# Optimization experiments

Hardware: AMD Instinct MI355X
Metric: run time of the kernel (lower is better)

The kernel has to match this reference:

```python
import jax, jax.numpy as jnp
import numpy as np
from jax import lax

INPUT_SIZE = 512
STRIDES = (8, 16, 32)
NUM_CLASSES = 2
KA = 3  # anchors per scale
EPS = 1e-8
ANCHORS = np.array([[[10, 13], [16, 30], [33, 23]],
                    [[30, 61], [62, 45], [59, 119]],
                    [[116, 90], [156, 198], [373, 326]]], dtype=np.float32)

def _grid(stride):
    f = INPUT_SIZE // stride
    gy, gx = np.meshgrid(np.arange(f), np.arange(f), indexing='ij')
    return jnp.asarray(np.stack([gx, gy], -1).reshape(-1, 2).astype(np.float32))  # [HW,2] (x,y)

GRIDS = [_grid(s) for s in STRIDES]


def conv_ltc(x, conv_w, bn_gamma, bn_beta, cm, vleak, tau_m, e_revin):
    """Discrete LTC recurrence over time (tau_input=True, usetaum=True, stream_opt=True).
    x: [B,T,C,H,W] -> [B,T,Cout,H,W]"""
    B, T, C, H, W = x.shape
    Cout = conv_w.shape[0]

    def step(v_pre, xt):
        z = lax.conv_general_dilated(xt, conv_w, (1, 1), ((1, 1), (1, 1)),
                                     dimension_numbers=('NCHW', 'OIHW', 'NCHW'))
        wih = z * bn_gamma + bn_beta  # BatchNorm in eval form (per-channel affine)
        num = tau_m * v_pre / (vleak + cm * jax.nn.sigmoid(wih)) + wih * e_revin
        v = jax.nn.sigmoid(num / (1.0 + EPS))
        return v, v

    v0 = jnp.zeros((B, Cout, H, W), x.dtype)
    _, ys = lax.scan(step, v0, jnp.moveaxis(x, 1, 0))  # [T,B,Cout,H,W]
    return jnp.moveaxis(ys, 0, 1)


def head(y, w, b):
    # 1x1 conv detection head
    return jnp.einsum('bchw,oc->bohw', y, w) + b[None, :, None, None]


def decode_scale(pred, i):
    """pred: [B, KA*(1+C+4), h, w] -> obj [B,hw*KA,1], cls [B,hw*KA,C], box [B,hw*KA,4]."""
    B, _, h, w = pred.shape
    s = STRIDES[i]
    p = jnp.transpose(pred, (0, 2, 3, 1))  # [B,h,w,21]
    obj = p[..., :KA].reshape(B, -1, 1)
    cls = p[..., KA:KA * (1 + NUM_CLASSES)].reshape(B, -1, NUM_CLASSES)
    reg = p[..., KA * (1 + NUM_CLASSES):].reshape(B, h * w, KA, 4)
    anchors = jnp.asarray(ANCHORS[i])  # [KA,2]
    xy = (jax.nn.sigmoid(reg[..., :2]) + GRIDS[i][None, :, None, :]) * s
    wh = jnp.exp(reg[..., 2:]) * anchors[None, None, :, :]
    xywh = jnp.concatenate([xy, wh], -1).reshape(B, -1, 4)
    box = jnp.concatenate([xywh[..., :2] - xywh[..., 2:] * 0.5,
                           xywh[..., :2] + xywh[..., 2:] * 0.5], -1) / INPUT_SIZE
    return obj, cls, box


def setup_inputs() -> dict:
    key = jax.random.key(0)
    ks = jax.random.split(key, 12)
    B = 8
    x = jax.random.uniform(ks[0], (B, 5, 5, 512, 512), jnp.float32)
    y1 = jax.random.normal(ks[1], (B, 768, 16, 16), jnp.float32)
    y2 = jax.random.normal(ks[2], (B, 384, 32, 32), jnp.float32)
    y3 = jax.random.normal(ks[3], (B, 192, 64, 64), jnp.float32)
    conv_w = jax.random.normal(ks[4], (5, 5, 3, 3), jnp.float32) * 0.15  # xavier-ish
    bn_gamma = jnp.ones((5, 1, 1), jnp.float32)
    bn_beta = jnp.zeros((5, 1, 1), jnp.float32)
    cm = 1.0 + 0.1 * jax.random.normal(ks[5], (5, 1, 1), jnp.float32)
    vleak = 1.0 + 0.1 * jax.random.normal(ks[6], (5, 1, 1), jnp.float32)
    tau_m = 0.8 - 0.3 * jax.random.uniform(ks[7], (5, 1, 1), jnp.float32)
    e_revin = 1.0 + 0.1 * jax.random.normal(ks[8], (5, 1, 1), jnp.float32)
    OC = KA * (1 + NUM_CLASSES + 4)  # 21
    w1 = jax.random.normal(ks[9], (OC, 768), jnp.float32) * 0.02
    w2 = jax.random.normal(ks[10], (OC, 384), jnp.float32) * 0.02
    w3 = jax.random.normal(ks[11], (OC, 192), jnp.float32) * 0.02
    b1 = jnp.zeros((OC,), jnp.float32)
    b2 = jnp.zeros((OC,), jnp.float32)
    b3 = jnp.zeros((OC,), jnp.float32)
    return dict(x=x, y1=y1, y2=y2, y3=y3, conv_w=conv_w, bn_gamma=bn_gamma,
                bn_beta=bn_beta, cm=cm, vleak=vleak, tau_m=tau_m, e_revin=e_revin,
                w1=w1, b1=b1, w2=w2, b2=b2, w3=w3, b3=b3)


def reference(x, y1, y2, y3, conv_w, bn_gamma, bn_beta, cm, vleak, tau_m, e_revin,
              w1, b1, w2, b2, w3, b3):
    enc = conv_ltc(x, conv_w, bn_gamma, bn_beta, cm, vleak, tau_m, e_revin)
    # preds ordered [pred_s (y3, stride 8), pred_m (y2, 16), pred_l (y1, 32)]
    preds = [head(y3, w3, b3), head(y2, w2, b2), head(y1, w1, b1)]
    objs, clss, boxes = [], [], []
    for i, p in enumerate(preds):
        o, c, bx = decode_scale(p, i)
        objs.append(o); clss.append(c); boxes.append(bx)
    det = jnp.concatenate([jnp.concatenate(objs, 1),
                           jnp.concatenate(clss, 1),
                           jnp.concatenate(boxes, 1)], -1)  # [B, 16128, 7]
    return enc, det
```

## Files before the change

kernel.cpp:

```cpp
#include <hip/hip_runtime.h>
#include <math.h>

#define HH 512
#define WW 512
#define HWp (HH * WW)
#define TT 5
#define CC 5

#define CTW 64
#define CTH 16
#define NROW (CTH + 2)
#define GCOL 18
#define LCP (GCOL * 4)
#define LDSF (CC * NROW * LCP)
#define NG (CC * NROW * GCOL)
#define NBUF 3
#define SPARE_BYTES (NBUF * LDSF * 4)

#define NHEADB 672
#define NCONVB 2048

#define XS_FLOATS (NBUF * LDSF + 256)

typedef float v2f __attribute__((ext_vector_type(2)));

typedef __attribute__((address_space(3))) char       lds_char_t;
typedef __attribute__((address_space(1)))  const char glb_char_t;

__device__ __forceinline__ float fast_sigmoid(float x) {
    return __builtin_amdgcn_rcpf(1.0f + __expf(-x));
}

extern "C" __global__ __launch_bounds__(512, 4)
void spikefpn_fused(const float* __restrict__ x, const float* __restrict__ cw,
                    const float* __restrict__ gamma, const float* __restrict__ beta,
                    const float* __restrict__ cm, const float* __restrict__ vleak,
                    const float* __restrict__ tau, const float* __restrict__ erev,
                    const float* __restrict__ y3, const float* __restrict__ w3, const float* __restrict__ b3,
                    const float* __restrict__ y2, const float* __restrict__ w2, const float* __restrict__ b2,
                    const float* __restrict__ y1, const float* __restrict__ w1, const float* __restrict__ b1,
                    float* __restrict__ out, float* __restrict__ det)
{
    __shared__ float xs[XS_FLOATS];

    const int bid = blockIdx.x;
    const int tid = threadIdx.x;

    if (bid < NHEADB) {
        float* smem = xs;
        const float *y, *w, *bias;
        int Cin, f, lgf, lgchunks, row_off;
        float s;
        float aw0, aw1, aw2, ah0, ah1, ah2;
        int sb;

        if (bid < 512) {
            sb = bid;       y = y3; w = w3; bias = b3; Cin = 192; f = 64; lgf = 6; lgchunks = 6; s = 8.0f;  row_off = 0;
            aw0 = 10.f;  ah0 = 13.f;  aw1 = 16.f;  ah1 = 30.f;  aw2 = 33.f;  ah2 = 23.f;
        } else if (bid < 640) {
            sb = bid - 512; y = y2; w = w2; bias = b2; Cin = 384; f = 32; lgf = 5; lgchunks = 4; s = 16.0f; row_off = 12288;
            aw0 = 30.f;  ah0 = 61.f;  aw1 = 62.f;  ah1 = 45.f;  aw2 = 59.f;  ah2 = 119.f;
        } else {
            sb = bid - 640; y = y1; w = w1; bias = b1; Cin = 768; f = 16; lgf = 4; lgchunks = 2; s = 32.0f; row_off = 15360;
            aw0 = 116.f; ah0 = 90.f;  aw1 = 156.f; ah1 = 198.f; aw2 = 373.f; ah2 = 326.f;
        }

        const int n     = f * f;
        const int b     = sb >> lgchunks;
        const int chunk = sb & ((1 << lgchunks) - 1);

        const int lane = tid & 63;
        const int grp  = tid >> 6;

        const int wtot = Cin * 21;
        for (int i = tid; i < wtot; i += 512) {
            int o = i / Cin;
            int c = i - o * Cin;
            smem[c * 24 + o] = w[i];
        }
        __syncthreads();

        const int G   = Cin >> 3;
        const int pix = (chunk << 6) + lane;

        float acc[21];
        #pragma unroll
        for (int o = 0; o < 21; ++o) acc[o] = 0.0f;

        const float* yp = y + ((size_t)b * Cin + (size_t)grp * G) * n + pix;
        const int wbase = grp * G * 24;

        #pragma unroll 4
        for (int c = 0; c < G; ++c) {
            float v = yp[(size_t)c * n];
            const float* wr = &smem[wbase + c * 24];
            float4 q0 = *(const float4*)(wr);
            float4 q1 = *(const float4*)(wr + 4);
            float4 q2 = *(const float4*)(wr + 8);
            float4 q3 = *(const float4*)(wr + 12);
            float4 q4 = *(const float4*)(wr + 16);
            float  s20 = wr[20];
            float wv[21] = {q0.x,q0.y,q0.z,q0.w, q1.x,q1.y,q1.z,q1.w,
                            q2.x,q2.y,q2.z,q2.w, q3.x,q3.y,q3.z,q3.w,
                            q4.x,q4.y,q4.z,q4.w, s20};
            #pragma unroll
            for (int o = 0; o < 21; ++o) acc[o] = fmaf(v, wv[o], acc[o]);
        }
        __syncthreads();

        #pragma unroll
        for (int o = 0; o < 21; ++o) smem[tid * 21 + o] = acc[o];
        __syncthreads();

        if (tid < 64) {
            float r[21];
            #pragma unroll
            for (int o = 0; o < 21; ++o) r[o] = bias[o];
            #pragma unroll
            for (int g2 = 0; g2 < 8; ++g2) {
                const float* rp = &smem[(g2 * 64 + lane) * 21];
                #pragma unroll
                for (int o = 0; o < 21; ++o) r[o] += rp[o];
            }

            const int hy = pix >> lgf;
            const int hx = pix & (f - 1);
            const float inv = 1.0f / 512.0f;
            const float AW[3] = {aw0, aw1, aw2};
            const float AH[3] = {ah0, ah1, ah2};

            #pragma unroll
            for (int a = 0; a < 3; ++a) {
                const int row = row_off + pix * 3 + a;
                float* dp = det + ((size_t)b * 16128 + row) * 7;
                dp[0] = r[a];
                dp[1] = r[3 + a * 2];
                dp[2] = r[4 + a * 2];
                float cx = (fast_sigmoid(r[9  + a * 4]) + (float)hx) * s;
                float cy = (fast_sigmoid(r[10 + a * 4]) + (float)hy) * s;
                float bw = __expf(r[11 + a * 4]) * AW[a];
                float bh = __expf(r[12 + a * 4]) * AH[a];
                dp[3] = (cx - bw * 0.5f) * inv;
                dp[4] = (cy - bh * 0.5f) * inv;
                dp[5] = (cx + bw * 0.5f) * inv;
                dp[6] = (cy + bh * 0.5f) * inv;
            }
        }
        return;
    }

    const int cb = bid - NHEADB;
    const int bx = cb & 7;
    const int by = (cb >> 3) & 31;
    const int b  = cb >> 8;

    const int grow0 = by * CTH;
    const int gcol0 = bx * CTW;
    const size_t xb = (size_t)b * (TT * CC * HWp);

    int  goff[4];
    bool pred[4];
    uint32_t gbase[4];
    #pragma unroll
    for (int k = 0; k < 4; ++k) {
        const int g = tid + k * 512;
        const int wavebase = (tid & ~63) + k * 512;
        if (wavebase >= NG) {
            pred[k] = true;
            goff[k] = 0;
            gbase[k] = (uint32_t)SPARE_BYTES;
        } else {
            const bool valid = g < NG;
            const int gg  = valid ? g : 0;
            const int ch  = gg / (NROW * GCOL);
            const int rem = gg - ch * (NROW * GCOL);
            const int row = rem / GCOL;
            const int c4  = rem - row * GCOL;
            const int gr = grow0 + row - 1;
            const int gc = gcol0 - 4 + c4 * 4;
            const bool inb = valid && ((unsigned)gr < (unsigned)HH) && ((unsigned)gc < (unsigned)WW);
            pred[k] = inb;
            goff[k] = ch * HWp + gr * WW + gc;
            gbase[k] = (uint32_t)(wavebase * 16);
            if (valid && !inb) {
                float4 z = make_float4(0.f, 0.f, 0.f, 0.f);
                *(float4*)&xs[g * 4]            = z;
                *(float4*)&xs[LDSF + g * 4]     = z;
                *(float4*)&xs[2 * LDSF + g * 4] = z;
            }
        }
    }

    lds_char_t* lds0 = (lds_char_t*)xs;

    auto issue_stage = [&](int t, int buf) {
        const float* xt = x + xb + (size_t)t * (CC * HWp);
        const uint32_t bufoff = (uint32_t)buf * (LDSF * 4);
        #pragma unroll
        for (int k = 0; k < 4; ++k) {
            if (pred[k]) {
                __builtin_amdgcn_global_load_lds(
                    (const __attribute__((address_space(1))) void*)(glb_char_t*)(const char*)(xt + goff[k]),
                    (__attribute__((address_space(3))) void*)(lds0 + bufoff + gbase[k]),
                    16, 0, 0);
            }
        }
    };

    float g_[CC], be[CC], cmv[CC], vl[CC], tm[CC], er[CC];
    #pragma unroll
    for (int o = 0; o < CC; ++o) {
        g_[o] = gamma[o]; be[o] = beta[o]; cmv[o] = cm[o];
        vl[o] = vleak[o]; tm[o] = tau[o]; er[o] = erev[o];
    }

    const int tx = tid & 63;
    const int r0 = (tid >> 6) * 2;

    issue_stage(0, 0);
    issue_stage(1, 1);
    asm volatile("s_waitcnt vmcnt(4)" ::: "memory");
    asm volatile("s_waitcnt lgkmcnt(0)" ::: "memory");
    __builtin_amdgcn_s_barrier();
    __builtin_amdgcn_sched_barrier(0);

    v2f vpre[CC];
    #pragma unroll
    for (int o = 0; o < CC; ++o) vpre[o] = (v2f){0.0f, 0.0f};

    #pragma unroll
    for (int t = 0; t < TT; ++t) {
        if (t + 2 < TT) issue_stage(t + 2, (t + 2) % NBUF);

        const float* cur = xs + (t % NBUF) * LDSF;

        v2f acc[CC];
        #pragma unroll
        for (int o = 0; o < CC; ++o) acc[o] = (v2f){0.0f, 0.0f};

        #pragma unroll
        for (int ic = 0; ic < CC; ++ic) {
            const float* lp = &cur[(ic * NROW + r0) * LCP + tx + 3];
            v2f xv[3][3];
            #pragma unroll
            for (int dr = 0; dr < 3; ++dr)
                #pragma unroll
                for (int dc = 0; dc < 3; ++dc)
                    xv[dr][dc] = (v2f){lp[dr * LCP + dc], lp[(dr + 1) * LCP + dc]};
            #pragma unroll
            for (int oc = 0; oc < CC; ++oc) {
                const float* wp = cw + (oc * CC + ic) * 9;
                v2f a = acc[oc];
                #pragma unroll
                for (int dr = 0; dr < 3; ++dr)
                    #pragma unroll
                    for (int dc = 0; dc < 3; ++dc) {
                        const float w = wp[dr * 3 + dc];
                        a = __builtin_elementwise_fma((v2f){w, w}, xv[dr][dc], a);
                    }
                acc[oc] = a;
            }
        }

        const size_t ob0 = (size_t)(grow0 + r0) * WW + gcol0 + tx;
        #pragma unroll
        for (int o = 0; o < CC; ++o) {
            float* op = out + ((size_t)((b * TT + t) * CC + o)) * HWp + ob0;

            float wih0 = fmaf(acc[o].x, g_[o], be[o]);
            float sg0  = fast_sigmoid(wih0);
            float den0 = fmaf(cmv[o], sg0, vl[o]);
            float num0 = fmaf(tm[o] * vpre[o].x, __builtin_amdgcn_rcpf(den0), wih0 * er[o]);
            float v0   = fast_sigmoid(num0);
            vpre[o].x = v0;
            op[0] = v0;

            float wih1 = fmaf(acc[o].y, g_[o], be[o]);
            float sg1  = fast_sigmoid(wih1);
            float den1 = fmaf(cmv[o], sg1, vl[o]);
            float num1 = fmaf(tm[o] * vpre[o].y, __builtin_amdgcn_rcpf(den1), wih1 * er[o]);
            float v1   = fast_sigmoid(num1);
            vpre[o].y = v1;
            op[WW] = v1;
        }

        if (t <= 2) {
            asm volatile("s_waitcnt vmcnt(14)" ::: "memory");
            __builtin_amdgcn_s_barrier();
            __builtin_amdgcn_sched_barrier(0);
        } else if (t == 3) {
            asm volatile("s_waitcnt vmcnt(10)" ::: "memory");
            __builtin_amdgcn_s_barrier();
            __builtin_amdgcn_sched_barrier(0);
        }
    }
}

extern "C" void kernel_launch(void* const* d_in, const int* in_sizes, int n_in,
                              void* d_out, int out_size, void* d_ws, size_t ws_size,
                              hipStream_t stream)
{
    const float* x     = (const float*)d_in[0];
    const float* y1    = (const float*)d_in[1];
    const float* y2    = (const float*)d_in[2];
    const float* y3    = (const float*)d_in[3];
    const float* cw    = (const float*)d_in[4];
    const float* gamma = (const float*)d_in[5];
    const float* beta  = (const float*)d_in[6];
    const float* cm    = (const float*)d_in[7];
    const float* vleak = (const float*)d_in[8];
    const float* tau   = (const float*)d_in[9];
    const float* erev  = (const float*)d_in[10];
    const float* w1    = (const float*)d_in[11];
    const float* b1    = (const float*)d_in[12];
    const float* w2    = (const float*)d_in[13];
    const float* b2    = (const float*)d_in[14];
    const float* w3    = (const float*)d_in[15];
    const float* b3    = (const float*)d_in[16];

    float* out = (float*)d_out;
    float* det = out + (size_t)8 * TT * CC * HH * WW;

    spikefpn_fused<<<dim3(NHEADB + NCONVB), 512, 0, stream>>>(
        x, cw, gamma, beta, cm, vleak, tau, erev,
        y3, w3, b3, y2, w2, b2, y1, w1, b1, out, det);
}
```

Measured before the change: 139.1 us.

## Process four batch items per conv block with a continuous cross-batch load pipeline

Each conv block now loops over four batch elements for the same spatial tile, cutting the conv grid from 2048 to 512 blocks. The triple-buffered global-to-LDS prefetch runs continuously across batch boundaries, so the pipeline fill at the start of each batch item disappears and per-block setup (offset computation, parameter loads, zero padding) is amortised. The trade-off is fewer blocks, which lowers parallelism and load balance across CUs, and the waitcnt sequence becomes more intricate.

```diff
diff --git a/kernel.cpp b/kernel.cpp
--- a/kernel.cpp
+++ b/kernel.cpp
@@ -18,9 +18,9 @@
 #define SPARE_BYTES (NBUF * LDSF * 4)
 
 #define NHEADB 672
-#define NCONVB 2048
-
-#define XS_FLOATS (NBUF * LDSF + 256)
+#define NCONVB 512
+
+#define LDS_TOTAL (NBUF * LDSF + 256)
 
 typedef float v2f __attribute__((ext_vector_type(2)));
 
@@ -41,7 +41,7 @@
                     const float* __restrict__ y1, const float* __restrict__ w1, const float* __restrict__ b1,
                     float* __restrict__ out, float* __restrict__ det)
 {
-    __shared__ float xs[XS_FLOATS];
+    __shared__ float xs[LDS_TOTAL];
 
     const int bid = blockIdx.x;
     const int tid = threadIdx.x;
@@ -152,11 +152,11 @@
     const int cb = bid - NHEADB;
     const int bx = cb & 7;
     const int by = (cb >> 3) & 31;
-    const int b  = cb >> 8;
+    const int bgrp = cb >> 8;
+    const int pbase = bgrp * 4 * TT * CC;
 
     const int grow0 = by * CTH;
     const int gcol0 = bx * CTW;
-    const size_t xb = (size_t)b * (TT * CC * HWp);
 
     int  goff[4];
     bool pred[4];
@@ -193,9 +193,9 @@
 
     lds_char_t* lds0 = (lds_char_t*)xs;
 
-    auto issue_stage = [&](int t, int buf) {
-        const float* xt = x + xb + (size_t)t * (CC * HWp);
-        const uint32_t bufoff = (uint32_t)buf * (LDSF * 4);
+    auto issue_stage = [&](int tau) {
+        const float* xt = x + (size_t)(pbase + tau * CC) * HWp;
+        const uint32_t bufoff = (uint32_t)(tau % NBUF) * (LDSF * 4);
         #pragma unroll
         for (int k = 0; k < 4; ++k) {
             if (pred[k]) {
@@ -217,81 +217,96 @@
     const int tx = tid & 63;
     const int r0 = (tid >> 6) * 2;
 
-    issue_stage(0, 0);
-    issue_stage(1, 1);
+    issue_stage(0);
+    issue_stage(1);
     asm volatile("s_waitcnt vmcnt(4)" ::: "memory");
     asm volatile("s_waitcnt lgkmcnt(0)" ::: "memory");
     __builtin_amdgcn_s_barrier();
     __builtin_amdgcn_sched_barrier(0);
 
-    v2f vpre[CC];
-    #pragma unroll
-    for (int o = 0; o < CC; ++o) vpre[o] = (v2f){0.0f, 0.0f};
-
-    #pragma unroll
-    for (int t = 0; t < TT; ++t) {
-        if (t + 2 < TT) issue_stage(t + 2, (t + 2) % NBUF);
-
-        const float* cur = xs + (t % NBUF) * LDSF;
-
-        v2f acc[CC];
-        #pragma unroll
-        for (int o = 0; o < CC; ++o) acc[o] = (v2f){0.0f, 0.0f};
-
-        #pragma unroll
-        for (int ic = 0; ic < CC; ++ic) {
-            const float* lp = &cur[(ic * NROW + r0) * LCP + tx + 3];
-            v2f xv[3][3];
-            #pragma unroll
-            for (int dr = 0; dr < 3; ++dr)
-                #pragma unroll
-                for (int dc = 0; dc < 3; ++dc)
-                    xv[dr][dc] = (v2f){lp[dr * LCP + dc], lp[(dr + 1) * LCP + dc]};
-            #pragma unroll
-            for (int oc = 0; oc < CC; ++oc) {
-                const float* wp = cw + (oc * CC + ic) * 9;
-                v2f a = acc[oc];
+    const size_t ob0 = (size_t)(grow0 + r0) * WW + gcol0 + tx;
+
+    #pragma unroll 1
+    for (int bb = 0; bb < 4; ++bb) {
+        v2f vpre[CC];
+        #pragma unroll
+        for (int o = 0; o < CC; ++o) vpre[o] = (v2f){0.0f, 0.0f};
+
+        #pragma unroll
+        for (int t = 0; t < TT; ++t) {
+            const int tau = bb * TT + t;
+            if (t < 3 || bb < 3) issue_stage(tau + 2);
+
+            const float* cur = xs + (tau % NBUF) * LDSF;
+
+            v2f acc[CC];
+            #pragma unroll
+            for (int o = 0; o < CC; ++o) acc[o] = (v2f){0.0f, 0.0f};
+
+            #pragma unroll
+            for (int ic = 0; ic < CC; ++ic) {
+                const float* lp = &cur[(ic * NROW + r0) * LCP + tx + 3];
+                v2f xv[3][3];
                 #pragma unroll
                 for (int dr = 0; dr < 3; ++dr)
                     #pragma unroll
-                    for (int dc = 0; dc < 3; ++dc) {
-                        const float w = wp[dr * 3 + dc];
-                        a = __builtin_elementwise_fma((v2f){w, w}, xv[dr][dc], a);
-                    }
-                acc[oc] = a;
-            }
-        }
-
-        const size_t ob0 = (size_t)(grow0 + r0) * WW + gcol0 + tx;
-        #pragma unroll
-        for (int o = 0; o < CC; ++o) {
-            float* op = out + ((size_t)((b * TT + t) * CC + o)) * HWp + ob0;
-
-            float wih0 = fmaf(acc[o].x, g_[o], be[o]);
-            float sg0  = fast_sigmoid(wih0);
-            float den0 = fmaf(cmv[o], sg0, vl[o]);
-            float num0 = fmaf(tm[o] * vpre[o].x, __builtin_amdgcn_rcpf(den0), wih0 * er[o]);
-            float v0   = fast_sigmoid(num0);
-            vpre[o].x = v0;
-            op[0] = v0;
-
-            float wih1 = fmaf(acc[o].y, g_[o], be[o]);
-            float sg1  = fast_sigmoid(wih1);
-            float den1 = fmaf(cmv[o], sg1, vl[o]);
-            float num1 = fmaf(tm[o] * vpre[o].y, __builtin_amdgcn_rcpf(den1), wih1 * er[o]);
-            float v1   = fast_sigmoid(num1);
-            vpre[o].y = v1;
-            op[WW] = v1;
-        }
-
-        if (t <= 2) {
-            asm volatile("s_waitcnt vmcnt(14)" ::: "memory");
-            __builtin_amdgcn_s_barrier();
-            __builtin_amdgcn_sched_barrier(0);
-        } else if (t == 3) {
-            asm volatile("s_waitcnt vmcnt(10)" ::: "memory");
-            __builtin_amdgcn_s_barrier();
-            __builtin_amdgcn_sched_barrier(0);
+                    for (int dc = 0; dc < 3; ++dc)
+                        xv[dr][dc] = (v2f){lp[dr * LCP + dc], lp[(dr + 1) * LCP + dc]};
+                #pragma unroll
+                for (int oc = 0; oc < CC; ++oc) {
+                    const float* wp = cw + (oc * CC + ic) * 9;
+                    v2f a = acc[oc];
+                    #pragma unroll
+                    for (int dr = 0; dr < 3; ++dr)
+                        #pragma unroll
+                        for (int dc = 0; dc < 3; ++dc) {
+                            const float w = wp[dr * 3 + dc];
+                            a = __builtin_elementwise_fma((v2f){w, w}, xv[dr][dc], a);
+                        }
+                    acc[oc] = a;
+                }
+            }
+
+            #pragma unroll
+            for (int o = 0; o < CC; ++o) {
+                float* op = out + (size_t)(pbase + tau * CC + o) * HWp + ob0;
+
+                float wih0 = fmaf(acc[o].x, g_[o], be[o]);
+                float sg0  = fast_sigmoid(wih0);
+                float den0 = fmaf(cmv[o], sg0, vl[o]);
+                float num0 = fmaf(tm[o] * vpre[o].x, __builtin_amdgcn_rcpf(den0), wih0 * er[o]);
+                float v0   = fast_sigmoid(num0);
+                vpre[o].x = v0;
+                op[0] = v0;
+
+                float wih1 = fmaf(acc[o].y, g_[o], be[o]);
+                float sg1  = fast_sigmoid(wih1);
+                float den1 = fmaf(cmv[o], sg1, vl[o]);
+                float num1 = fmaf(tm[o] * vpre[o].y, __builtin_amdgcn_rcpf(den1), wih1 * er[o]);
+                float v1   = fast_sigmoid(num1);
+                vpre[o].y = v1;
+                op[WW] = v1;
+            }
+
+            if (t < 3) {
+                asm volatile("s_waitcnt vmcnt(14)" ::: "memory");
+                __builtin_amdgcn_s_barrier();
+                __builtin_amdgcn_sched_barrier(0);
+            } else if (t == 3) {
+                if (bb < 3) {
+                    asm volatile("s_waitcnt vmcnt(14)" ::: "memory");
+                } else {
+                    asm volatile("s_waitcnt vmcnt(10)" ::: "memory");
+                }
+                __builtin_amdgcn_s_barrier();
+                __builtin_amdgcn_sched_barrier(0);
+            } else {
+                if (bb < 3) {
+                    asm volatile("s_waitcnt vmcnt(14)" ::: "memory");
+                    __builtin_amdgcn_s_barrier();
+                    __builtin_amdgcn_sched_barrier(0);
+                }
+            }
         }
     }
 }
```

After: 175.4 us. +26.0%, slower.
